# Kernel optimization log

Hardware: AMD Instinct MI355X
Metric: run time of the kernel (lower is better)

Reference implementation:

```python
import jax, jax.numpy as jnp
import numpy as np

B, S, D = 2, 2048, 1024
H = 16
DH = D // H  # 64


def setup_inputs() -> dict:
    key = jax.random.key(0)
    k1, k2, k3 = jax.random.split(key, 3)
    x = jax.random.normal(k1, (B, S, D), dtype=jnp.float32)
    W_qkv = jax.random.normal(k2, (D, 3 * D), dtype=jnp.float32) * 0.01
    b_qkv = jnp.zeros((3 * D,), dtype=jnp.float32)
    W_out = jax.random.normal(k3, (D, D), dtype=jnp.float32) * 0.01
    b_out = jnp.zeros((D,), dtype=jnp.float32)
    return {"x": x, "W_qkv": W_qkv, "b_qkv": b_qkv, "W_out": W_out, "b_out": b_out}


def reference(x, W_qkv, b_qkv, W_out, b_out):
    b, s, d = x.shape
    h, dh = H, DH
    # fused QKV projection
    qkv = x @ W_qkv + b_qkv                       # [b, s, 3d]
    qkv = qkv.reshape(b, s, 3, h, dh)
    q, k, v = qkv[:, :, 0], qkv[:, :, 1], qkv[:, :, 2]  # [b, s, h, dh]
    q = q.transpose(0, 2, 1, 3)                    # [b, h, s, dh]
    k = k.transpose(0, 2, 1, 3)
    v = v.transpose(0, 2, 1, 3)
    inv_sqrt_d = jnp.asarray(1.0 / np.sqrt(dh), dtype=x.dtype)
    scores = jnp.einsum('bhqd,bhkd->bhqk', q, k) * inv_sqrt_d  # [b, h, s, s]
    causal = jnp.tril(jnp.ones((s, s), dtype=bool))[None, None]
    # source masks with -10000.0 (not -inf)
    scores = jnp.where(causal, scores, jnp.asarray(-10000.0, dtype=scores.dtype))
    probs = jax.nn.softmax(scores, axis=-1)
    attn = jnp.einsum('bhqk,bhkd->bhqd', probs, v)  # [b, h, s, dh]
    attn = attn.transpose(0, 2, 1, 3).reshape(b, s, d)
    return attn @ W_out + b_out
```

## Files before the change

kernel.cpp:

```cpp
#include <hip/hip_runtime.h>
#include <hip/hip_bf16.h>

#define B_  2
#define S_  2048
#define D_  1024
#define H_  16
#define DH_ 64
#define M_  (B_ * S_)
#define QKV_LD (3 * D_)

typedef __bf16 bf16x8 __attribute__((ext_vector_type(8)));
typedef float  f32x4  __attribute__((ext_vector_type(4)));
typedef unsigned short us4 __attribute__((ext_vector_type(4)));
typedef unsigned short us8 __attribute__((ext_vector_type(8)));

__device__ inline unsigned short f2bf(float f) {
  union { __bf16 h; unsigned short u; } cv; cv.h = (__bf16)f; return cv.u;
}
__device__ inline float bf2f(unsigned short u) {
  union { unsigned int i; float f; } cv; cv.i = ((unsigned int)u) << 16; return cv.f;
}
__device__ inline unsigned int pk2bf(float lo, float hi) {
  return (unsigned int)f2bf(lo) | ((unsigned int)f2bf(hi) << 16);
}
__device__ inline void cstore(float* p, float v) { *p = v; }
__device__ inline void cstore(unsigned short* p, float v) { *p = f2bf(v); }

__device__ inline void gload_lds16(const void* g, void* lds) {
  __builtin_amdgcn_global_load_lds(
      (const __attribute__((address_space(1))) unsigned int*)g,
      (__attribute__((address_space(3))) unsigned int*)lds, 16, 0, 0);
}

__global__ __launch_bounds__(256) void prep_all(
    const float* __restrict__ x, unsigned short* __restrict__ x_bf,
    const float* __restrict__ W_qkv, unsigned short* __restrict__ wqkvT,
    const float* __restrict__ W_out, unsigned short* __restrict__ woutT) {
  __shared__ float tile[32][33];
  const int blk = blockIdx.x;
  const int t = threadIdx.x;
  if (blk < 4096) {
    int i = blk * 256 + t;
    float4 v = ((const float4*)x)[i];
    us4 p = { f2bf(v.x), f2bf(v.y), f2bf(v.z), f2bf(v.w) };
    ((us4*)x_bf)[i] = p;
    return;
  }
  const float* W; unsigned short* Wt; int K, N, bi;
  if (blk < 4096 + 3072) { bi = blk - 4096; W = W_qkv; Wt = wqkvT; K = D_; N = QKV_LD; }
  else                   { bi = blk - 7168; W = W_out; Wt = woutT; K = D_; N = D_; }
  const int bx = bi % (N / 32), by = bi / (N / 32);
  const int tx = t & 31, ty = t >> 5;
  const int c0 = bx * 32, r0 = by * 32;
  #pragma unroll
  for (int i = 0; i < 4; ++i)
    tile[ty + 8 * i][tx] = W[(size_t)(r0 + ty + 8 * i) * N + c0 + tx];
  __syncthreads();
  #pragma unroll
  for (int i = 0; i < 4; ++i)
    Wt[(size_t)(c0 + ty + 8 * i) * K + r0 + tx] = f2bf(tile[tx][ty + 8 * i]);
}

template<typename CT>
__global__ __launch_bounds__(256) void gemm_bf16_tn(
    const unsigned short* __restrict__ A,
    const unsigned short* __restrict__ Bt,
    const float* __restrict__ bias,
    CT* __restrict__ C, int N, int K) {
  __shared__ __align__(16) unsigned short smA[128 * 32];
  __shared__ __align__(16) unsigned short smB[128 * 32];
  const int t = threadIdx.x;
  const int w = t >> 6, l = t & 63;
  const int lg = l >> 4, lr = l & 15;
  const int nwg  = gridDim.x * gridDim.y;
  const int bid0 = blockIdx.y * gridDim.x + blockIdx.x;
  const int swz  = (bid0 & 7) * (nwg >> 3) + (bid0 >> 3);
  const int bx = swz % gridDim.x, by = swz / gridDim.x;
  const int row0 = by * 128, col0 = bx * 128;
  const int wm = (w >> 1) * 64, wn = (w & 1) * 64;

  f32x4 acc[4][4] = {};

  for (int k0 = 0; k0 < K; k0 += 32) {
    __syncthreads();
    #pragma unroll
    for (int i = 0; i < 2; ++i) {
      const int inst = 2 * w + i;
      const int r = inst * 16 + (l >> 2);
      const int cb = (l & 3) * 8;
      gload_lds16(A  + (size_t)(row0 + r) * K + k0 + cb, &smA[inst * 512]);
      gload_lds16(Bt + (size_t)(col0 + r) * K + k0 + cb, &smB[inst * 512]);
    }
    __syncthreads();

    bf16x8 af[4], bfr[4];
    #pragma unroll
    for (int m = 0; m < 4; ++m)
      af[m] = *(const bf16x8*)&smA[(wm + m * 16 + lr) * 32 + lg * 8];
    #pragma unroll
    for (int n = 0; n < 4; ++n)
      bfr[n] = *(const bf16x8*)&smB[(wn + n * 16 + lr) * 32 + lg * 8];
    #pragma unroll
    for (int m = 0; m < 4; ++m)
      #pragma unroll
      for (int n = 0; n < 4; ++n)
        acc[m][n] = __builtin_amdgcn_mfma_f32_16x16x32_bf16(af[m], bfr[n], acc[m][n], 0, 0, 0);
  }

  #pragma unroll
  for (int m = 0; m < 4; ++m) {
    #pragma unroll
    for (int n = 0; n < 4; ++n) {
      const int col = col0 + wn + n * 16 + lr;
      const float bv = bias[col];
      #pragma unroll
      for (int r = 0; r < 4; ++r) {
        const int row = row0 + wm + m * 16 + lg * 4 + r;
        cstore(&C[(size_t)row * N + col], acc[m][n][r] + bv);
      }
    }
  }
}

__global__ __launch_bounds__(512, 4) void attn_fwd_mfma(
    const unsigned short* __restrict__ qkv, unsigned short* __restrict__ attn_out) {
  const int bid = blockIdx.x;
  const int xcd = bid & 7;
  const int li  = bid >> 3;
  const int bh  = xcd * 4 + (li >> 4);
  const int x   = li & 15;
  const int b = bh / H_, h = bh % H_;
  const unsigned short* base = qkv + (size_t)b * S_ * QKV_LD;

  __shared__ __align__(16) char smK[2][64 * 128];
  __shared__ __align__(16) char smV[2][64 * 128];

  const int t  = threadIdx.x;
  const int w  = t >> 6;
  const bool lo = (w < 4);
  const int wq = w & 3;
  const int l  = t & 63;
  const int lg = l >> 4;
  const int lr = l & 15;

  const int qt  = lo ? x : (31 - x);
  const int qw0 = qt * 64 + wq * 16;

  const unsigned short* kbase = base + D_ + h * DH_;
  const unsigned short* vbase = base + 2 * D_ + h * DH_;

  us8 kreg[2], vreg[2];
  const int kp  = (t & 31) * 2;
  const int vdb = ((t >> 5) & 7) * 8;

  auto issue_loads = [&](int k0) {
    #pragma unroll
    for (int it = 0; it < 2; ++it) {
      int idx = t + it * 256;
      int r = idx >> 3, c = idx & 7;
      kreg[it] = *(const us8*)(kbase + (size_t)(k0 + r) * QKV_LD + c * 8);
    }
    vreg[0] = *(const us8*)(vbase + (size_t)(k0 + kp) * QKV_LD + vdb);
    vreg[1] = *(const us8*)(vbase + (size_t)(k0 + kp + 1) * QKV_LD + vdb);
  };
  auto write_lds = [&](int buf) {
    #pragma unroll
    for (int it = 0; it < 2; ++it) {
      int idx = t + it * 256;
      int r = idx >> 3, c = idx & 7;
      int rho = (r & 0x23) | ((r & 0x04) << 2) | ((r & 0x18) >> 1);
      *(us8*)(smK[buf] + rho * 128 + ((c * 16) ^ ((rho & 7) << 4))) = kreg[it];
    }
    #pragma unroll
    for (int j = 0; j < 8; ++j) {
      int row = vdb + j;
      unsigned int pv = (unsigned int)vreg[0][j] | ((unsigned int)vreg[1][j] << 16);
      *(unsigned int*)(smV[buf] + row * 128 + ((2 * kp) ^ ((row & 7) << 4))) = pv;
    }
  };

  bf16x8 qf[2];
  {
    const unsigned short* qp = base + (size_t)(qw0 + lr) * QKV_LD + h * DH_ + 8 * lg;
    #pragma unroll
    for (int ks = 0; ks < 2; ++ks) {
      us8 qv = *(const us8*)(qp + 32 * ks);
      #pragma unroll
      for (int e = 0; e < 8; ++e) qf[ks][e] = (__bf16)(bf2f(qv[e]) * 0.18033688f);
    }
  }

  float mrun = -1e30f, lrun = 0.f;
  f32x4 acc_o[4] = {};

  const int ntiles = 32 - x;
  if (t < 256) { issue_loads(0); write_lds(0); }
  __syncthreads();

  for (int kti = 0; kti < ntiles; ++kti) {
    const int k0 = kti * 64;
    const int cur = kti & 1;

    if (t < 256 && kti + 1 < ntiles) issue_loads((kti + 1) * 64);

    const bool active = lo ? (kti <= x) : true;
    if (active) {
      f32x4 sc[4] = {};
      #pragma unroll
      for (int kt = 0; kt < 4; ++kt)
        #pragma unroll
        for (int ks = 0; ks < 2; ++ks) {
          int row = kt * 16 + lr;
          bf16x8 kb_ = *(const bf16x8*)(smK[cur] + row * 128 +
                                        (((ks * 64) + 16 * lg) ^ ((row & 7) << 4)));
          sc[kt] = __builtin_amdgcn_mfma_f32_16x16x32_bf16(kb_, qf[ks], sc[kt], 0, 0, 0);
        }

      if (k0 + 63 > qw0) {
        #pragma unroll
        for (int kt = 0; kt < 4; ++kt)
          #pragma unroll
          for (int r = 0; r < 4; ++r) {
            int kc = k0 + ((kt >> 1) << 5) + (lg << 3) + ((kt & 1) << 2) + r;
            if (kc > qw0 + lr) sc[kt][r] = -1e30f;
          }
      }

      float v = fmaxf(fmaxf(sc[0][0], sc[0][1]), fmaxf(sc[0][2], sc[0][3]));
      #pragma unroll
      for (int kt = 1; kt < 4; ++kt)
        v = fmaxf(v, fmaxf(fmaxf(sc[kt][0], sc[kt][1]), fmaxf(sc[kt][2], sc[kt][3])));
      v = fmaxf(v, __shfl_xor(v, 16));
      v = fmaxf(v, __shfl_xor(v, 32));
      if (!__all(v <= mrun + 8.0f)) {
        const float mnew = fmaxf(mrun, v);
        const float alpha = exp2f(mrun - mnew);
        mrun = mnew;
        float alphaO[4];
        #pragma unroll
        for (int r = 0; r < 4; ++r)
          alphaO[r] = __shfl(alpha, (l & 48) | (lg * 4 + r));
        #pragma unroll
        for (int dt = 0; dt < 4; ++dt)
          #pragma unroll
          for (int r = 0; r < 4; ++r) acc_o[dt][r] *= alphaO[r];
        lrun *= alpha;
      }
      float s = 0.f;
      #pragma unroll
      for (int kt = 0; kt < 4; ++kt)
        #pragma unroll
        for (int r = 0; r < 4; ++r) {
          float p = exp2f(sc[kt][r] - mrun);
          sc[kt][r] = p;
          s += p;
        }
      s += __shfl_xor(s, 16);
      s += __shfl_xor(s, 32);
      lrun += s;

      union { unsigned int u[4]; bf16x8 v8; } pa[2];
      #pragma unroll
      for (int ks = 0; ks < 2; ++ks) {
        pa[ks].u[0] = pk2bf(sc[2 * ks][0], sc[2 * ks][1]);
        pa[ks].u[1] = pk2bf(sc[2 * ks][2], sc[2 * ks][3]);
        pa[ks].u[2] = pk2bf(sc[2 * ks + 1][0], sc[2 * ks + 1][1]);
        pa[ks].u[3] = pk2bf(sc[2 * ks + 1][2], sc[2 * ks + 1][3]);
      }

      #pragma unroll
      for (int dt = 0; dt < 4; ++dt)
        #pragma unroll
        for (int ks = 0; ks < 2; ++ks) {
          int row = dt * 16 + lr;
          bf16x8 vb = *(const bf16x8*)(smV[cur] + row * 128 +
                                       (((ks * 64) + 16 * lg) ^ ((row & 7) << 4)));
          acc_o[dt] = __builtin_amdgcn_mfma_f32_16x16x32_bf16(pa[ks].v8, vb, acc_o[dt], 0, 0, 0);
        }
    }

    if (t < 256 && kti + 1 < ntiles) write_lds(cur ^ 1);
    __syncthreads();
  }

  const float inv = 1.0f / lrun;
  float invO[4];
  #pragma unroll
  for (int r = 0; r < 4; ++r)
    invO[r] = __shfl(inv, (l & 48) | (lg * 4 + r));
  #pragma unroll
  for (int dt = 0; dt < 4; ++dt)
    #pragma unroll
    for (int r = 0; r < 4; ++r)
      attn_out[(size_t)(b * S_ + qw0 + lg * 4 + r) * D_ + h * DH_ + dt * 16 + lr] =
          f2bf(acc_o[dt][r] * invO[r]);
}

extern "C" void kernel_launch(void* const* d_in, const int* in_sizes, int n_in,
                              void* d_out, int out_size, void* d_ws, size_t ws_size,
                              hipStream_t stream) {
  const float* x     = (const float*)d_in[0];
  const float* W_qkv = (const float*)d_in[1];
  const float* b_qkv = (const float*)d_in[2];
  const float* W_out = (const float*)d_in[3];
  const float* b_out = (const float*)d_in[4];
  float* out = (float*)d_out;

  char* ws = (char*)d_ws;
  unsigned short* qkv_bf  = (unsigned short*)ws;  ws += (size_t)M_ * QKV_LD * 2;
  unsigned short* attn_bf = (unsigned short*)ws;  ws += (size_t)M_ * D_ * 2;
  unsigned short* x_bf    = (unsigned short*)ws;  ws += (size_t)M_ * D_ * 2;
  unsigned short* wqkvT   = (unsigned short*)ws;  ws += (size_t)QKV_LD * D_ * 2;
  unsigned short* woutT   = (unsigned short*)ws;

  dim3 blk(256);
  prep_all<<<4096 + 3072 + 1024, blk, 0, stream>>>(x, x_bf, W_qkv, wqkvT, W_out, woutT);
  gemm_bf16_tn<unsigned short><<<dim3(QKV_LD / 128, M_ / 128), blk, 0, stream>>>(
      x_bf, wqkvT, b_qkv, qkv_bf, QKV_LD, D_);
  attn_fwd_mfma<<<dim3(512), dim3(512), 0, stream>>>(qkv_bf, attn_bf);
  gemm_bf16_tn<float><<<dim3(D_ / 128, M_ / 128), blk, 0, stream>>>(
      attn_bf, woutT, b_out, out, D_, D_);
}
```

Before: 122.4 us.

## Process both causal-paired query tiles per wave to share K/V fragment loads

Each attention block now uses 4 waves instead of 8, and each wave handles both the low and high query tiles of the causal pair. Each K and V fragment read from LDS is reused for two MFMAs, and all threads take part in the global-to-LDS staging. This removes the idle low-half waves in late tiles and halves LDS reads per MFMA. In exchange it roughly doubles register use per wave (two accumulators, two softmax states), lowers the launch bound to 256 threads with 2 blocks, and cuts the number of resident waves.

```diff
diff --git a/kernel.cpp b/kernel.cpp
--- a/kernel.cpp
+++ b/kernel.cpp
@@ -122,7 +122,7 @@
   }
 }
 
-__global__ __launch_bounds__(512, 4) void attn_fwd_mfma(
+__global__ __launch_bounds__(256, 2) void attn_fwd_mfma(
     const unsigned short* __restrict__ qkv, unsigned short* __restrict__ attn_out) {
   const int bid = blockIdx.x;
   const int xcd = bid & 7;
@@ -136,15 +136,13 @@
   __shared__ __align__(16) char smV[2][64 * 128];
 
   const int t  = threadIdx.x;
-  const int w  = t >> 6;
-  const bool lo = (w < 4);
-  const int wq = w & 3;
+  const int wq = t >> 6;
   const int l  = t & 63;
   const int lg = l >> 4;
   const int lr = l & 15;
 
-  const int qt  = lo ? x : (31 - x);
-  const int qw0 = qt * 64 + wq * 16;
+  const int qlo0 = 64 * x + wq * 16;
+  const int qhi0 = 64 * (31 - x) + wq * 16;
 
   const unsigned short* kbase = base + D_ + h * DH_;
   const unsigned short* vbase = base + 2 * D_ + h * DH_;
@@ -179,121 +177,156 @@
     }
   };
 
-  bf16x8 qf[2];
-  {
-    const unsigned short* qp = base + (size_t)(qw0 + lr) * QKV_LD + h * DH_ + 8 * lg;
+  bf16x8 qflo[2], qfhi[2];
+  #pragma unroll
+  for (int p = 0; p < 2; ++p) {
+    const int q0 = p ? qhi0 : qlo0;
+    const unsigned short* qp = base + (size_t)(q0 + lr) * QKV_LD + h * DH_ + 8 * lg;
     #pragma unroll
     for (int ks = 0; ks < 2; ++ks) {
       us8 qv = *(const us8*)(qp + 32 * ks);
       #pragma unroll
-      for (int e = 0; e < 8; ++e) qf[ks][e] = (__bf16)(bf2f(qv[e]) * 0.18033688f);
-    }
-  }
-
-  float mrun = -1e30f, lrun = 0.f;
-  f32x4 acc_o[4] = {};
+      for (int e = 0; e < 8; ++e)
+        (p ? qfhi : qflo)[ks][e] = (__bf16)(bf2f(qv[e]) * 0.18033688f);
+    }
+  }
+
+  float mlo = -1e30f, llo = 0.f;
+  float mhi = -1e30f, lhi = 0.f;
+  f32x4 alo[4] = {}, ahi[4] = {};
+
+  auto softmax_pack = [&](f32x4 (&sc)[4], float& mrun, float& lrun,
+                          f32x4 (&acc)[4], unsigned int (&pau)[2][4]) {
+    float v = fmaxf(fmaxf(sc[0][0], sc[0][1]), fmaxf(sc[0][2], sc[0][3]));
+    #pragma unroll
+    for (int kt = 1; kt < 4; ++kt)
+      v = fmaxf(v, fmaxf(fmaxf(sc[kt][0], sc[kt][1]), fmaxf(sc[kt][2], sc[kt][3])));
+    v = fmaxf(v, __shfl_xor(v, 16));
+    v = fmaxf(v, __shfl_xor(v, 32));
+    if (!__all(v <= mrun + 8.0f)) {
+      const float mnew = fmaxf(mrun, v);
+      const float alpha = exp2f(mrun - mnew);
+      mrun = mnew;
+      float alphaO[4];
+      #pragma unroll
+      for (int r = 0; r < 4; ++r)
+        alphaO[r] = __shfl(alpha, (l & 48) | (lg * 4 + r));
+      #pragma unroll
+      for (int dt = 0; dt < 4; ++dt)
+        #pragma unroll
+        for (int r = 0; r < 4; ++r) acc[dt][r] *= alphaO[r];
+      lrun *= alpha;
+    }
+    float s = 0.f;
+    #pragma unroll
+    for (int kt = 0; kt < 4; ++kt)
+      #pragma unroll
+      for (int r = 0; r < 4; ++r) {
+        float p = exp2f(sc[kt][r] - mrun);
+        sc[kt][r] = p;
+        s += p;
+      }
+    s += __shfl_xor(s, 16);
+    s += __shfl_xor(s, 32);
+    lrun += s;
+    #pragma unroll
+    for (int ks = 0; ks < 2; ++ks) {
+      pau[ks][0] = pk2bf(sc[2 * ks][0], sc[2 * ks][1]);
+      pau[ks][1] = pk2bf(sc[2 * ks][2], sc[2 * ks][3]);
+      pau[ks][2] = pk2bf(sc[2 * ks + 1][0], sc[2 * ks + 1][1]);
+      pau[ks][3] = pk2bf(sc[2 * ks + 1][2], sc[2 * ks + 1][3]);
+    }
+  };
 
   const int ntiles = 32 - x;
-  if (t < 256) { issue_loads(0); write_lds(0); }
+  issue_loads(0);
+  write_lds(0);
   __syncthreads();
 
   for (int kti = 0; kti < ntiles; ++kti) {
     const int k0 = kti * 64;
     const int cur = kti & 1;
-
-    if (t < 256 && kti + 1 < ntiles) issue_loads((kti + 1) * 64);
-
-    const bool active = lo ? (kti <= x) : true;
-    if (active) {
-      f32x4 sc[4] = {};
-      #pragma unroll
-      for (int kt = 0; kt < 4; ++kt)
-        #pragma unroll
-        for (int ks = 0; ks < 2; ++ks) {
-          int row = kt * 16 + lr;
-          bf16x8 kb_ = *(const bf16x8*)(smK[cur] + row * 128 +
-                                        (((ks * 64) + 16 * lg) ^ ((row & 7) << 4)));
-          sc[kt] = __builtin_amdgcn_mfma_f32_16x16x32_bf16(kb_, qf[ks], sc[kt], 0, 0, 0);
-        }
-
-      if (k0 + 63 > qw0) {
-        #pragma unroll
-        for (int kt = 0; kt < 4; ++kt)
-          #pragma unroll
-          for (int r = 0; r < 4; ++r) {
-            int kc = k0 + ((kt >> 1) << 5) + (lg << 3) + ((kt & 1) << 2) + r;
-            if (kc > qw0 + lr) sc[kt][r] = -1e30f;
-          }
-      }
-
-      float v = fmaxf(fmaxf(sc[0][0], sc[0][1]), fmaxf(sc[0][2], sc[0][3]));
-      #pragma unroll
-      for (int kt = 1; kt < 4; ++kt)
-        v = fmaxf(v, fmaxf(fmaxf(sc[kt][0], sc[kt][1]), fmaxf(sc[kt][2], sc[kt][3])));
-      v = fmaxf(v, __shfl_xor(v, 16));
-      v = fmaxf(v, __shfl_xor(v, 32));
-      if (!__all(v <= mrun + 8.0f)) {
-        const float mnew = fmaxf(mrun, v);
-        const float alpha = exp2f(mrun - mnew);
-        mrun = mnew;
-        float alphaO[4];
-        #pragma unroll
-        for (int r = 0; r < 4; ++r)
-          alphaO[r] = __shfl(alpha, (l & 48) | (lg * 4 + r));
-        #pragma unroll
-        for (int dt = 0; dt < 4; ++dt)
-          #pragma unroll
-          for (int r = 0; r < 4; ++r) acc_o[dt][r] *= alphaO[r];
-        lrun *= alpha;
-      }
-      float s = 0.f;
+    const bool lo_act = (kti <= x);
+
+    if (kti + 1 < ntiles) issue_loads((kti + 1) * 64);
+
+    f32x4 schi[4], sclo[4];
+    #pragma unroll
+    for (int kt = 0; kt < 4; ++kt) {
+      schi[kt] = f32x4{0.f, 0.f, 0.f, 0.f};
+      sclo[kt] = f32x4{0.f, 0.f, 0.f, 0.f};
+      #pragma unroll
+      for (int ks = 0; ks < 2; ++ks) {
+        int row = kt * 16 + lr;
+        bf16x8 kb_ = *(const bf16x8*)(smK[cur] + row * 128 +
+                                      (((ks * 64) + 16 * lg) ^ ((row & 7) << 4)));
+        schi[kt] = __builtin_amdgcn_mfma_f32_16x16x32_bf16(kb_, qfhi[ks], schi[kt], 0, 0, 0);
+        if (lo_act)
+          sclo[kt] = __builtin_amdgcn_mfma_f32_16x16x32_bf16(kb_, qflo[ks], sclo[kt], 0, 0, 0);
+      }
+    }
+
+    if (kti == ntiles - 1) {
       #pragma unroll
       for (int kt = 0; kt < 4; ++kt)
         #pragma unroll
         for (int r = 0; r < 4; ++r) {
-          float p = exp2f(sc[kt][r] - mrun);
-          sc[kt][r] = p;
-          s += p;
+          int kc = k0 + ((kt >> 1) << 5) + (lg << 3) + ((kt & 1) << 2) + r;
+          if (kc > qhi0 + lr) schi[kt][r] = -1e30f;
         }
-      s += __shfl_xor(s, 16);
-      s += __shfl_xor(s, 32);
-      lrun += s;
-
-      union { unsigned int u[4]; bf16x8 v8; } pa[2];
+    }
+    if (lo_act && kti == x) {
+      #pragma unroll
+      for (int kt = 0; kt < 4; ++kt)
+        #pragma unroll
+        for (int r = 0; r < 4; ++r) {
+          int kc = k0 + ((kt >> 1) << 5) + (lg << 3) + ((kt & 1) << 2) + r;
+          if (kc > qlo0 + lr) sclo[kt][r] = -1e30f;
+        }
+    }
+
+    unsigned int pahi[2][4], palo[2][4];
+    softmax_pack(schi, mhi, lhi, ahi, pahi);
+    if (lo_act) softmax_pack(sclo, mlo, llo, alo, palo);
+
+    #pragma unroll
+    for (int dt = 0; dt < 4; ++dt)
       #pragma unroll
       for (int ks = 0; ks < 2; ++ks) {
-        pa[ks].u[0] = pk2bf(sc[2 * ks][0], sc[2 * ks][1]);
-        pa[ks].u[1] = pk2bf(sc[2 * ks][2], sc[2 * ks][3]);
-        pa[ks].u[2] = pk2bf(sc[2 * ks + 1][0], sc[2 * ks + 1][1]);
-        pa[ks].u[3] = pk2bf(sc[2 * ks + 1][2], sc[2 * ks + 1][3]);
-      }
-
-      #pragma unroll
-      for (int dt = 0; dt < 4; ++dt)
-        #pragma unroll
-        for (int ks = 0; ks < 2; ++ks) {
-          int row = dt * 16 + lr;
-          bf16x8 vb = *(const bf16x8*)(smV[cur] + row * 128 +
-                                       (((ks * 64) + 16 * lg) ^ ((row & 7) << 4)));
-          acc_o[dt] = __builtin_amdgcn_mfma_f32_16x16x32_bf16(pa[ks].v8, vb, acc_o[dt], 0, 0, 0);
+        int row = dt * 16 + lr;
+        bf16x8 vb = *(const bf16x8*)(smV[cur] + row * 128 +
+                                     (((ks * 64) + 16 * lg) ^ ((row & 7) << 4)));
+        union { unsigned int u[4]; bf16x8 v8; } ph, pl;
+        ph.u[0] = pahi[ks][0]; ph.u[1] = pahi[ks][1];
+        ph.u[2] = pahi[ks][2]; ph.u[3] = pahi[ks][3];
+        ahi[dt] = __builtin_amdgcn_mfma_f32_16x16x32_bf16(ph.v8, vb, ahi[dt], 0, 0, 0);
+        if (lo_act) {
+          pl.u[0] = palo[ks][0]; pl.u[1] = palo[ks][1];
+          pl.u[2] = palo[ks][2]; pl.u[3] = palo[ks][3];
+          alo[dt] = __builtin_amdgcn_mfma_f32_16x16x32_bf16(pl.v8, vb, alo[dt], 0, 0, 0);
         }
-    }
-
-    if (t < 256 && kti + 1 < ntiles) write_lds(cur ^ 1);
+      }
+
+    if (kti + 1 < ntiles) write_lds(cur ^ 1);
     __syncthreads();
   }
 
-  const float inv = 1.0f / lrun;
-  float invO[4];
-  #pragma unroll
-  for (int r = 0; r < 4; ++r)
-    invO[r] = __shfl(inv, (l & 48) | (lg * 4 + r));
-  #pragma unroll
-  for (int dt = 0; dt < 4; ++dt)
+  #pragma unroll
+  for (int p = 0; p < 2; ++p) {
+    const int q0 = p ? qhi0 : qlo0;
+    const float inv = 1.0f / (p ? lhi : llo);
+    float invO[4];
     #pragma unroll
     for (int r = 0; r < 4; ++r)
-      attn_out[(size_t)(b * S_ + qw0 + lg * 4 + r) * D_ + h * DH_ + dt * 16 + lr] =
-          f2bf(acc_o[dt][r] * invO[r]);
+      invO[r] = __shfl(inv, (l & 48) | (lg * 4 + r));
+    #pragma unroll
+    for (int dt = 0; dt < 4; ++dt)
+      #pragma unroll
+      for (int r = 0; r < 4; ++r) {
+        float vv = (p ? ahi : alo)[dt][r] * invO[r];
+        attn_out[(size_t)(b * S_ + q0 + lg * 4 + r) * D_ + h * DH_ + dt * 16 + lr] = f2bf(vv);
+      }
+  }
 }
 
 extern "C" void kernel_launch(void* const* d_in, const int* in_sizes, int n_in,
@@ -317,7 +350,7 @@
   prep_all<<<4096 + 3072 + 1024, blk, 0, stream>>>(x, x_bf, W_qkv, wqkvT, W_out, woutT);
   gemm_bf16_tn<unsigned short><<<dim3(QKV_LD / 128, M_ / 128), blk, 0, stream>>>(
       x_bf, wqkvT, b_qkv, qkv_bf, QKV_LD, D_);
-  attn_fwd_mfma<<<dim3(512), dim3(512), 0, stream>>>(qkv_bf, attn_bf);
+  attn_fwd_mfma<<<dim3(512), dim3(256), 0, stream>>>(qkv_bf, attn_bf);
   gemm_bf16_tn<float><<<dim3(D_ / 128, M_ / 128), blk, 0, stream>>>(
       attn_bf, woutT, b_out, out, D_, D_);
 }
```

After: 133.0 us. 1.09x slower.
